# Optimization experiments

Hardware: AMD Instinct MI355X
Metric: run time of the kernel (lower is better)

The kernel has to match this reference:

```python
import jax, jax.numpy as jnp
import numpy as np

N_HEADS = 16
D_MODEL = 1024
NEG_INF = float('-inf')


def _rope_tables(seq_len, d_k, dtype):
    # RoPE(dim=d_k//2): Theta_i = 10000^(-i/dim), repeat-interleaved to width d_k;
    # positions start at 1 (torch uses arange(1, max_len+1)).
    dim = d_k // 2
    theta = jnp.exp(-jnp.arange(dim, dtype=dtype) * (np.log(10000.0) / dim))
    theta = jnp.repeat(theta, 2)                      # [d_k]
    pos = jnp.arange(1, seq_len + 1, dtype=dtype)[:, None]  # [S,1]
    ang = pos * theta                                 # [S,d_k]
    return jnp.sin(ang), jnp.cos(ang)


def _rope(x):
    # x: [B,H,S,d_k]; pair rotation (x0,x1)->(-x1,x0), Rx = x*cos + rot(x)*sin
    B, H, S, d_k = x.shape
    sin, cos = _rope_tables(S, d_k, x.dtype)
    xp = x.reshape(B, H, S, d_k // 2, 2)
    rot = jnp.stack([-xp[..., 1], xp[..., 0]], axis=-1).reshape(x.shape)
    return x * cos + rot * sin


def setup_inputs() -> dict:
    key = jax.random.key(0)
    ks = jax.random.split(key, 8)
    B, S, D, H = 2, 1024, D_MODEL, N_HEADS
    source_query = jax.random.normal(ks[0], (B, S, D), dtype=jnp.float32)
    source_key_value = jax.random.normal(ks[1], (B, S, D), dtype=jnp.float32)
    # tail padding: lengths in [820, 1024]
    q_len = jax.random.randint(ks[2], (B,), 820, S + 1)
    kv_len = jax.random.randint(ks[3], (B,), 820, S + 1)
    pos = jnp.arange(S)
    source_query_padding_mask = pos[None, :] >= q_len[:, None]    # True = pad
    source_key_value_padding_mask = pos[None, :] >= kv_len[:, None]
    prev = jax.random.normal(ks[4], (1, B, H, S, S), dtype=jnp.float32) * 0.5
    Wq = jax.random.normal(ks[5], (D, D), dtype=jnp.float32) * 0.02
    Wk = jax.random.normal(ks[6], (D, D), dtype=jnp.float32) * 0.02
    kv2 = jax.random.split(ks[7], 2)
    Wv = jax.random.normal(kv2[0], (D, D), dtype=jnp.float32) * 0.02
    Wproj = jax.random.normal(kv2[1], (D, D), dtype=jnp.float32) * 0.02
    return dict(source_query=source_query, source_key_value=source_key_value,
                source_query_padding_mask=source_query_padding_mask,
                source_key_value_padding_mask=source_key_value_padding_mask,
                prev=prev, Wq=Wq, Wk=Wk, Wv=Wv, Wproj=Wproj)


def reference(source_query, source_key_value, source_query_padding_mask,
              source_key_value_padding_mask, prev, Wq, Wk, Wv, Wproj):
    B, Sq, D = source_query.shape
    Sk = source_key_value.shape[1]
    H = N_HEADS
    d_k = D // H

    def split_heads(x, S):
        return x.reshape(B, S, H, d_k).transpose(0, 2, 1, 3)  # [B,H,S,d_k]

    # nn.Linear(bias=False): y = x @ W.T
    q = split_heads(jnp.einsum('bsd,ed->bse', source_query, Wq), Sq)
    k = split_heads(jnp.einsum('bsd,ed->bse', source_key_value, Wk), Sk)
    v = split_heads(jnp.einsum('bsd,ed->bse', source_key_value, Wv), Sk)

    q = _rope(q)
    k = _rope(k)

    scores = jnp.einsum('bhqd,bhkd->bhqk', q, k) * (d_k ** -0.5)
    q_pad = source_query_padding_mask[:, None, :, None]   # [B,1,Sq,1]
    kv_pad = source_key_value_padding_mask[:, None, None, :]  # [B,1,1,Sk]
    scores = jnp.where(q_pad, NEG_INF, scores)
    scores = jnp.where(kv_pad, NEG_INF, scores)
    causal = jnp.tril(jnp.ones((Sq, Sq), dtype=bool))      # masked=True
    scores = jnp.where(causal, scores, NEG_INF)

    prev_new = jnp.concatenate([prev, scores[None]], axis=0)  # [L+1,B,H,Sq,Sk]
    avg = prev_new.mean(0)

    # rows fully -inf (padded queries) would softmax to NaN in torch, then get
    # filled with 0 -> compute a safe softmax and zero those rows instead.
    safe = jnp.where(q_pad, 0.0, avg)
    w = jax.nn.softmax(safe, axis=-1)
    w = jnp.where(q_pad, 0.0, w)

    attn = jnp.einsum('bhqk,bhkd->bhqd', w, v)
    attn = attn.transpose(0, 2, 1, 3).reshape(B, Sq, D)
    out = jnp.einsum('bsd,ed->bse', attn, Wproj)  # dropout=0 (eval)
    return out, prev_new
```

## Files before the change

kernel.cpp:

```cpp
#include <hip/hip_runtime.h>
#include <math.h>

#define NSEQ 1024
#define NH   16
#define DKH  64

#define NEGBIG (-1.0e30f)

typedef unsigned short u16;
typedef unsigned int   u32;
typedef __attribute__((ext_vector_type(8))) short short8;
typedef __attribute__((ext_vector_type(4))) float f32x4;

__global__ __launch_bounds__(256) void normalize_masks(
    const unsigned char* __restrict__ qm, const unsigned char* __restrict__ km,
    int* __restrict__ outq, int* __restrict__ outk)
{
    __shared__ int flag;
    if (threadIdx.x == 0) flag = 0;
    __syncthreads();
    int f = 0;
    for (int i = threadIdx.x; i < 2048; i += 256) {
        if ((i & 3) && qm[i]) f = 1;
        if ((i & 3) && km[i]) f = 1;
    }
    if (f) atomicOr(&flag, 1);
    __syncthreads();
    const int isbyte = flag;
    for (int i = threadIdx.x; i < 2048; i += 256) {
        outq[i] = isbyte ? (int)qm[i] : ((const int*)qm)[i];
        outk[i] = isbyte ? (int)km[i] : ((const int*)km)[i];
    }
}

__device__ __forceinline__ u32 bf16_rn(float x) {
    u32 u = __float_as_uint(x);
    return (u + 0x7FFFu + ((u >> 16) & 1u)) >> 16;
}
__device__ __forceinline__ void bf16_split(float x, u32 &h, u32 &l) {
    h = bf16_rn(x);
    l = bf16_rn(x - __uint_as_float(h << 16));
}

__device__ __forceinline__ void mfma_core(
    const float* __restrict__ X, const float* __restrict__ W,
    u16 (*Ahi)[40], u16 (*Alo)[40], u16 (*Bhi)[40], u16 (*Blo)[40],
    f32x4 (&acc)[4][2], int m0, int e0, int tid)
{
    const int lane = tid & 63, wid = tid >> 6;
    const int wm = wid >> 1, wn = wid & 1;
    const int l15 = lane & 15, lq = lane >> 4;
    const int arow = tid >> 1, aks = (tid & 1) * 16;
    const int brow = tid >> 2, bks = (tid & 3) * 8;
    const float* aptr = &X[(size_t)(m0 + arow) * 1024 + aks];
    const float* bptr = &W[(size_t)(e0 + brow) * 1024 + bks];

    float4 xa[4], xb[2];
    #pragma unroll
    for (int c = 0; c < 4; ++c) xa[c] = *(const float4*)(aptr + 4 * c);
    #pragma unroll
    for (int c = 0; c < 2; ++c) xb[c] = *(const float4*)(bptr + 4 * c);

    for (int k0 = 0; k0 < 1024; k0 += 32) {
        u32 pah[8], pal[8], pbh[4], pbl[4];
        #pragma unroll
        for (int c = 0; c < 4; ++c) {
            u32 h0, l0, h1, l1, h2, l2, h3, l3;
            bf16_split(xa[c].x, h0, l0); bf16_split(xa[c].y, h1, l1);
            bf16_split(xa[c].z, h2, l2); bf16_split(xa[c].w, h3, l3);
            pah[2 * c] = h0 | (h1 << 16); pah[2 * c + 1] = h2 | (h3 << 16);
            pal[2 * c] = l0 | (l1 << 16); pal[2 * c + 1] = l2 | (l3 << 16);
        }
        #pragma unroll
        for (int c = 0; c < 2; ++c) {
            u32 h0, l0, h1, l1, h2, l2, h3, l3;
            bf16_split(xb[c].x, h0, l0); bf16_split(xb[c].y, h1, l1);
            bf16_split(xb[c].z, h2, l2); bf16_split(xb[c].w, h3, l3);
            pbh[2 * c] = h0 | (h1 << 16); pbh[2 * c + 1] = h2 | (h3 << 16);
            pbl[2 * c] = l0 | (l1 << 16); pbl[2 * c + 1] = l2 | (l3 << 16);
        }
        __syncthreads();
        *(uint4*)&Ahi[arow][aks]     = make_uint4(pah[0], pah[1], pah[2], pah[3]);
        *(uint4*)&Ahi[arow][aks + 8] = make_uint4(pah[4], pah[5], pah[6], pah[7]);
        *(uint4*)&Alo[arow][aks]     = make_uint4(pal[0], pal[1], pal[2], pal[3]);
        *(uint4*)&Alo[arow][aks + 8] = make_uint4(pal[4], pal[5], pal[6], pal[7]);
        *(uint4*)&Bhi[brow][bks]     = make_uint4(pbh[0], pbh[1], pbh[2], pbh[3]);
        *(uint4*)&Blo[brow][bks]     = make_uint4(pbl[0], pbl[1], pbl[2], pbl[3]);
        __syncthreads();
        if (k0 + 32 < 1024) {
            #pragma unroll
            for (int c = 0; c < 4; ++c) xa[c] = *(const float4*)(aptr + k0 + 32 + 4 * c);
            #pragma unroll
            for (int c = 0; c < 2; ++c) xb[c] = *(const float4*)(bptr + k0 + 32 + 4 * c);
        }
        short8 bh8[2], bl8[2];
        #pragma unroll
        for (int fn = 0; fn < 2; ++fn) {
            const int bc = wn * 32 + fn * 16 + l15;
            bh8[fn] = *(const short8*)&Bhi[bc][lq * 8];
            bl8[fn] = *(const short8*)&Blo[bc][lq * 8];
        }
        #pragma unroll
        for (int fm = 0; fm < 4; ++fm) {
            const int ar = wm * 64 + fm * 16 + l15;
            short8 ah8 = *(const short8*)&Ahi[ar][lq * 8];
            short8 al8 = *(const short8*)&Alo[ar][lq * 8];
            #pragma unroll
            for (int fn = 0; fn < 2; ++fn) {
                acc[fm][fn] = __builtin_amdgcn_mfma_f32_16x16x32_bf16(ah8, bh8[fn], acc[fm][fn], 0, 0, 0);
                acc[fm][fn] = __builtin_amdgcn_mfma_f32_16x16x32_bf16(ah8, bl8[fn], acc[fm][fn], 0, 0, 0);
                acc[fm][fn] = __builtin_amdgcn_mfma_f32_16x16x32_bf16(al8, bh8[fn], acc[fm][fn], 0, 0, 0);
            }
        }
    }
}

__global__ __launch_bounds__(256) void gemm_qkv(
    const float* __restrict__ srcq, const float* __restrict__ srckv,
    const float* __restrict__ Wq, const float* __restrict__ Wk,
    const float* __restrict__ Wv,
    float* __restrict__ qh, float* __restrict__ kh, float* __restrict__ vh)
{
    __shared__ __align__(16) u16 Ahi[128][40];
    __shared__ __align__(16) u16 Alo[128][40];
    __shared__ __align__(16) u16 Bhi[64][40];
    __shared__ __align__(16) u16 Blo[64][40];
    const int tid = threadIdx.x;
    const int z = blockIdx.z;
    const float* X = (z == 0) ? srcq : srckv;
    const float* W = (z == 0) ? Wq : (z == 1) ? Wk : Wv;
    float* Y       = (z == 0) ? qh : (z == 1) ? kh : vh;
    const int m0 = blockIdx.y * 128, e0 = blockIdx.x * 64;

    f32x4 acc[4][2];
    #pragma unroll
    for (int i = 0; i < 4; ++i)
        #pragma unroll
        for (int j = 0; j < 2; ++j) acc[i][j] = (f32x4){0.f, 0.f, 0.f, 0.f};

    mfma_core(X, W, Ahi, Alo, Bhi, Blo, acc, m0, e0, tid);

    const int lane = tid & 63, wid = tid >> 6;
    const int wm = wid >> 1, wn = wid & 1;
    const int l15 = lane & 15, lq = lane >> 4;
    const bool rope = (z != 2);
    const float cth = 0.28782313662425575f;
    float th[2];
    #pragma unroll
    for (int fn = 0; fn < 2; ++fn) {
        const int e = e0 + wn * 32 + fn * 16 + l15;
        th[fn] = rope ? expf(-(float)((e & 63) >> 1) * cth) : 0.f;
    }
    #pragma unroll
    for (int fm = 0; fm < 4; ++fm) {
        #pragma unroll
        for (int r = 0; r < 4; ++r) {
            const int m = m0 + wm * 64 + fm * 16 + lq * 4 + r;
            const int b = m >> 10, s = m & 1023;
            const float pos = (float)(s + 1);
            #pragma unroll
            for (int fn = 0; fn < 2; ++fn) {
                const int e = e0 + wn * 32 + fn * 16 + l15;
                float v = acc[fm][fn][r];
                const float vp = __shfl_xor(v, 1);
                if (rope) {
                    float sp, cp;
                    sincosf(pos * th[fn], &sp, &cp);
                    v = (lane & 1) ? (v * cp + vp * sp) : (v * cp - vp * sp);
                }
                const int h = e >> 6, db = e & 63;
                Y[(((size_t)(b * NH + h) << 10) + s) * DKH + db] = v;
            }
        }
    }
}

__global__ __launch_bounds__(256) void gemm_proj(
    const float* __restrict__ X, const float* __restrict__ W,
    float* __restrict__ Y)
{
    __shared__ __align__(16) u16 Ahi[128][40];
    __shared__ __align__(16) u16 Alo[128][40];
    __shared__ __align__(16) u16 Bhi[64][40];
    __shared__ __align__(16) u16 Blo[64][40];
    const int tid = threadIdx.x;
    const int m0 = blockIdx.y * 128, e0 = blockIdx.x * 64;

    f32x4 acc[4][2];
    #pragma unroll
    for (int i = 0; i < 4; ++i)
        #pragma unroll
        for (int j = 0; j < 2; ++j) acc[i][j] = (f32x4){0.f, 0.f, 0.f, 0.f};

    mfma_core(X, W, Ahi, Alo, Bhi, Blo, acc, m0, e0, tid);

    const int lane = tid & 63, wid = tid >> 6;
    const int wm = wid >> 1, wn = wid & 1;
    const int l15 = lane & 15, lq = lane >> 4;
    #pragma unroll
    for (int fm = 0; fm < 4; ++fm) {
        #pragma unroll
        for (int fn = 0; fn < 2; ++fn) {
            #pragma unroll
            for (int r = 0; r < 4; ++r) {
                const int row = m0 + wm * 64 + fm * 16 + lq * 4 + r;
                const int col = e0 + wn * 32 + fn * 16 + l15;
                Y[(size_t)row * 1024 + col] = acc[fm][fn][r];
            }
        }
    }
}

__global__ __launch_bounds__(256) void flash_fused(
    const float* __restrict__ qh, const float* __restrict__ kh,
    const float* __restrict__ vh, const float* __restrict__ prev,
    const int* __restrict__ nmq, const int* __restrict__ nmk,
    float* __restrict__ prevc, float* __restrict__ scb,
    float* __restrict__ attn)
{
    const int bh = blockIdx.y;
    const int b = bh >> 4, h = bh & 15;
    const int bx = blockIdx.x;
    const int qt = (bx & 1) ? (15 - (bx >> 1)) : (bx >> 1);
    const int q0 = qt * 64;
    const int tid = threadIdx.x;
    const int ti = tid >> 4, tj = tid & 15;
    const int r0 = ti * 4, c0 = tj * 4;
    const size_t base = ((size_t)bh << 10) * 1024;
    const float NI = NEGBIG;

    __shared__ float Qs[64][68];
    __shared__ float KW[64][68];
    __shared__ float Vs[64][68];

    const int lr = tid >> 2;
    const int ld0 = (tid & 3) * 4;
    {
        const float* qbase = qh + (((size_t)bh << 10) + q0) * DKH;
        #pragma unroll
        for (int dq = 0; dq < 4; ++dq) {
            const int d0 = ld0 + dq * 16;
            float4 qv = *(const float4*)&qbase[(size_t)lr * DKH + d0];
            Qs[d0 + 0][lr] = qv.x; Qs[d0 + 1][lr] = qv.y;
            Qs[d0 + 2][lr] = qv.z; Qs[d0 + 3][lr] = qv.w;
        }
    }

    {
        const float4 ninf4 = make_float4(NI, NI, NI, NI);
        for (int kt = qt + 1; kt < 16; ++kt) {
            const int k0 = kt * 64;
            #pragma unroll
            for (int u = 0; u < 4; ++u) {
                const int e = u * 256 + tid;
                const int rr = e >> 4, cc = (e & 15) * 4;
                const size_t idx = base + (size_t)(q0 + rr) * 1024 + k0 + cc;
                *(float4*)&prevc[idx] = *(const float4*)&prev[idx];
                *(float4*)&scb[idx] = ninf4;
            }
        }
    }

    int qmv[4];
    #pragma unroll
    for (int i = 0; i < 4; ++i) qmv[i] = nmq[(b << 10) + q0 + r0 + i];

    float m_i[4], l_i[4], O[4][4];
    #pragma unroll
    for (int i = 0; i < 4; ++i) {
        m_i[i] = -3.0e38f; l_i[i] = 0.f;
        #pragma unroll
        for (int j = 0; j < 4; ++j) O[i][j] = 0.f;
    }

    const float* kbase = kh + ((size_t)bh << 10) * DKH;
    const float* vbase = vh + ((size_t)bh << 10) * DKH;

    for (int kt = 0; kt <= qt; ++kt) {
        const int k0 = kt * 64;
        __syncthreads();

        #pragma unroll
        for (int dq = 0; dq < 4; ++dq) {
            const int d0 = ld0 + dq * 16;
            float4 kv4 = *(const float4*)&kbase[(size_t)(k0 + lr) * DKH + d0];
            KW[d0 + 0][lr] = kv4.x; KW[d0 + 1][lr] = kv4.y;
            KW[d0 + 2][lr] = kv4.z; KW[d0 + 3][lr] = kv4.w;
        }
        #pragma unroll
        for (int u = 0; u < 4; ++u) {
            const int e = u * 256 + tid;
            const int kv = e >> 4, dd = (e & 15) * 4;
            *(float4*)&Vs[kv][dd] =
                *(const float4*)&vbase[(size_t)(k0 + kv) * DKH + dd];
        }
        __syncthreads();

        float acc[4][4] = {{0.f}};
        #pragma unroll 8
        for (int d = 0; d < 64; ++d) {
            float a[4], bb[4];
            *(float4*)a  = *(const float4*)&Qs[d][r0];
            *(float4*)bb = *(const float4*)&KW[d][c0];
            #pragma unroll
            for (int i = 0; i < 4; ++i)
                #pragma unroll
                for (int j = 0; j < 4; ++j)
                    acc[i][j] += a[i] * bb[j];
        }

        int km[4];
        #pragma unroll
        for (int j = 0; j < 4; ++j) km[j] = nmk[(b << 10) + k0 + c0 + j];
        float aw[4][4], tmx[4];
        #pragma unroll
        for (int i = 0; i < 4; ++i) {
            const int row = q0 + r0 + i;
            float o[4];
            #pragma unroll
            for (int j = 0; j < 4; ++j) {
                const int col = k0 + c0 + j;
                const bool masked = (col > row) || (qmv[i] != 0) || (km[j] != 0);
                o[j] = masked ? NI : acc[i][j] * 0.125f;
            }
            const size_t idx = base + (size_t)row * 1024 + k0 + c0;
            *(float4*)&scb[idx] = make_float4(o[0], o[1], o[2], o[3]);
            const float4 p4 = *(const float4*)&prev[idx];
            *(float4*)&prevc[idx] = p4;
            aw[i][0] = 0.5f * (p4.x + o[0]);
            aw[i][1] = 0.5f * (p4.y + o[1]);
            aw[i][2] = 0.5f * (p4.z + o[2]);
            aw[i][3] = 0.5f * (p4.w + o[3]);
            tmx[i] = fmaxf(fmaxf(aw[i][0], aw[i][1]), fmaxf(aw[i][2], aw[i][3]));
        }
        #pragma unroll
        for (int i = 0; i < 4; ++i)
            #pragma unroll
            for (int off = 1; off < 16; off <<= 1)
                tmx[i] = fmaxf(tmx[i], __shfl_xor(tmx[i], off));

        __syncthreads();

        #pragma unroll
        for (int i = 0; i < 4; ++i) {
            const float mn = fmaxf(m_i[i], tmx[i]);
            const float fac = expf(m_i[i] - mn);
            m_i[i] = mn;
            float w0 = expf(aw[i][0] - mn);
            float w1 = expf(aw[i][1] - mn);
            float w2 = expf(aw[i][2] - mn);
            float w3 = expf(aw[i][3] - mn);
            float sl = w0 + w1 + w2 + w3;
            #pragma unroll
            for (int off = 1; off < 16; off <<= 1)
                sl += __shfl_xor(sl, off);
            l_i[i] = l_i[i] * fac + sl;
            #pragma unroll
            for (int j = 0; j < 4; ++j) O[i][j] *= fac;
            KW[c0 + 0][r0 + i] = w0;
            KW[c0 + 1][r0 + i] = w1;
            KW[c0 + 2][r0 + i] = w2;
            KW[c0 + 3][r0 + i] = w3;
        }
        __syncthreads();

        #pragma unroll 8
        for (int k = 0; k < 64; ++k) {
            float wv[4], vv[4];
            *(float4*)wv = *(const float4*)&KW[k][r0];
            *(float4*)vv = *(const float4*)&Vs[k][c0];
            #pragma unroll
            for (int i = 0; i < 4; ++i)
                #pragma unroll
                for (int j = 0; j < 4; ++j)
                    O[i][j] += wv[i] * vv[j];
        }
    }

    #pragma unroll
    for (int i = 0; i < 4; ++i) {
        const int q = q0 + r0 + i;
        const float inv = qmv[i] ? 0.f : 1.f / l_i[i];
        float4 o4 = make_float4(O[i][0] * inv, O[i][1] * inv,
                                O[i][2] * inv, O[i][3] * inv);
        *(float4*)&attn[(size_t)((b << 10) + q) * 1024 + (h << 6) + c0] = o4;
    }
}

extern "C" void kernel_launch(void* const* d_in, const int* in_sizes, int n_in,
                              void* d_out, int out_size, void* d_ws, size_t ws_size,
                              hipStream_t stream) {
    const float* srcq  = (const float*)d_in[0];
    const float* srckv = (const float*)d_in[1];
    const void*  qmask = d_in[2];
    const void*  kmask = d_in[3];
    const float* prev  = (const float*)d_in[4];
    const float* Wq    = (const float*)d_in[5];
    const float* Wk    = (const float*)d_in[6];
    const float* Wv    = (const float*)d_in[7];
    const float* Wp    = (const float*)d_in[8];

    float* out0  = (float*)d_out;
    float* prevc = out0 + 2097152;
    float* scb   = prevc + 33554432;

    float* qh   = (float*)d_ws;
    float* kh   = qh + 2097152;
    float* vh   = kh + 2097152;
    float* attn = vh + 2097152;
    int*   nmq  = (int*)(attn + 2097152);
    int*   nmk  = nmq + 2048;

    hipLaunchKernelGGL(normalize_masks, dim3(1), dim3(256), 0, stream,
                       (const unsigned char*)qmask, (const unsigned char*)kmask, nmq, nmk);
    hipLaunchKernelGGL(gemm_qkv, dim3(16, 16, 3), dim3(256), 0, stream,
                       srcq, srckv, Wq, Wk, Wv, qh, kh, vh);
    hipLaunchKernelGGL(flash_fused, dim3(16, 32), dim3(256), 0, stream,
                       qh, kh, vh, prev, nmq, nmk, prevc, scb, attn);
    hipLaunchKernelGGL(gemm_proj, dim3(16, 16), dim3(256), 0, stream,
                       attn, Wp, out0);
}
```

Baseline: 596.9 us.

## Pre-split inputs to bf16 hi/lo and move prev copy into a standalone kernel

Adds a pre-pass kernel that splits the activations and all four weight matrices into bf16 hi/lo arrays once. The GEMMs then load ready-made bf16 data instead of redoing the split in every tile, which removes repeated conversion work per block. The attention kernel now writes its output directly as bf16 hi/lo for the projection GEMM. The copy of prev into the output, and the fill of the fully masked upper blocks, move into a separate grid-stride kernel, so the fused attention kernel no longer carries that streaming traffic. The costs are extra kernel launches, more workspace, and a second full read of prev: once in the copy kernel and again in the attention kernel.

Result: slower. 648.0 us (+8.6%).

```diff
diff --git a/kernel.cpp b/kernel.cpp
--- a/kernel.cpp
+++ b/kernel.cpp
@@ -42,8 +42,56 @@
     l = bf16_rn(x - __uint_as_float(h << 16));
 }
 
+__global__ __launch_bounds__(256) void split_bf16(
+    const float* __restrict__ srcq, const float* __restrict__ srckv,
+    const float* __restrict__ Wq, const float* __restrict__ Wk,
+    const float* __restrict__ Wv, const float* __restrict__ Wp,
+    u16* __restrict__ sqh, u16* __restrict__ sql,
+    u16* __restrict__ skvh, u16* __restrict__ skvl,
+    u16* __restrict__ w4h, u16* __restrict__ w4l)
+{
+    const int z = blockIdx.z;
+    const float* src; u16 *dh, *dl; int n;
+    if (z == 0)      { src = srcq;  dh = sqh;  dl = sql;  n = 1 << 21; }
+    else if (z == 1) { src = srckv; dh = skvh; dl = skvl; n = 1 << 21; }
+    else {
+        src = (z == 2) ? Wq : (z == 3) ? Wk : (z == 4) ? Wv : Wp;
+        dh = w4h + ((size_t)(z - 2) << 20);
+        dl = w4l + ((size_t)(z - 2) << 20);
+        n = 1 << 20;
+    }
+    const int i8 = (blockIdx.x * 256 + threadIdx.x) * 8;
+    if (i8 >= n) return;
+    const float4 a = *(const float4*)&src[i8];
+    const float4 b = *(const float4*)&src[i8 + 4];
+    const float v[8] = {a.x, a.y, a.z, a.w, b.x, b.y, b.z, b.w};
+    u32 h[8], l[8];
+    #pragma unroll
+    for (int j = 0; j < 8; ++j) bf16_split(v[j], h[j], l[j]);
+    *(uint4*)&dh[i8] = make_uint4(h[0] | (h[1] << 16), h[2] | (h[3] << 16),
+                                  h[4] | (h[5] << 16), h[6] | (h[7] << 16));
+    *(uint4*)&dl[i8] = make_uint4(l[0] | (l[1] << 16), l[2] | (l[3] << 16),
+                                  l[4] | (l[5] << 16), l[6] | (l[7] << 16));
+}
+
+__global__ __launch_bounds__(256) void full_copy(
+    const float* __restrict__ prev, float* __restrict__ prevc,
+    float* __restrict__ scb)
+{
+    const float4 n4 = make_float4(NEGBIG, NEGBIG, NEGBIG, NEGBIG);
+    for (unsigned i = blockIdx.x * 256 + threadIdx.x; i < (1u << 23); i += gridDim.x * 256) {
+        const size_t e = (size_t)i * 4;
+        const float4 p = *(const float4*)&prev[e];
+        *(float4*)&prevc[e] = p;
+        const int q = (int)((e >> 10) & 1023);
+        const int k = (int)(e & 1023);
+        if ((k >> 6) > (q >> 6)) *(float4*)&scb[e] = n4;
+    }
+}
+
 __device__ __forceinline__ void mfma_core(
-    const float* __restrict__ X, const float* __restrict__ W,
+    const u16* __restrict__ Xhi, const u16* __restrict__ Xlo,
+    const u16* __restrict__ Whi, const u16* __restrict__ Wlo,
     u16 (*Ahi)[40], u16 (*Alo)[40], u16 (*Bhi)[40], u16 (*Blo)[40],
     f32x4 (&acc)[4][2], int m0, int e0, int tid)
 {
@@ -52,46 +100,34 @@
     const int l15 = lane & 15, lq = lane >> 4;
     const int arow = tid >> 1, aks = (tid & 1) * 16;
     const int brow = tid >> 2, bks = (tid & 3) * 8;
-    const float* aptr = &X[(size_t)(m0 + arow) * 1024 + aks];
-    const float* bptr = &W[(size_t)(e0 + brow) * 1024 + bks];
-
-    float4 xa[4], xb[2];
-    #pragma unroll
-    for (int c = 0; c < 4; ++c) xa[c] = *(const float4*)(aptr + 4 * c);
-    #pragma unroll
-    for (int c = 0; c < 2; ++c) xb[c] = *(const float4*)(bptr + 4 * c);
+    const u16* axh = &Xhi[(size_t)(m0 + arow) * 1024 + aks];
+    const u16* axl = &Xlo[(size_t)(m0 + arow) * 1024 + aks];
+    const u16* bxh = &Whi[(size_t)(e0 + brow) * 1024 + bks];
+    const u16* bxl = &Wlo[(size_t)(e0 + brow) * 1024 + bks];
+
+    uint4 rah0 = *(const uint4*)axh;
+    uint4 rah1 = *(const uint4*)(axh + 8);
+    uint4 ral0 = *(const uint4*)axl;
+    uint4 ral1 = *(const uint4*)(axl + 8);
+    uint4 rbh  = *(const uint4*)bxh;
+    uint4 rbl  = *(const uint4*)bxl;
 
     for (int k0 = 0; k0 < 1024; k0 += 32) {
-        u32 pah[8], pal[8], pbh[4], pbl[4];
-        #pragma unroll
-        for (int c = 0; c < 4; ++c) {
-            u32 h0, l0, h1, l1, h2, l2, h3, l3;
-            bf16_split(xa[c].x, h0, l0); bf16_split(xa[c].y, h1, l1);
-            bf16_split(xa[c].z, h2, l2); bf16_split(xa[c].w, h3, l3);
-            pah[2 * c] = h0 | (h1 << 16); pah[2 * c + 1] = h2 | (h3 << 16);
-            pal[2 * c] = l0 | (l1 << 16); pal[2 * c + 1] = l2 | (l3 << 16);
-        }
-        #pragma unroll
-        for (int c = 0; c < 2; ++c) {
-            u32 h0, l0, h1, l1, h2, l2, h3, l3;
-            bf16_split(xb[c].x, h0, l0); bf16_split(xb[c].y, h1, l1);
-            bf16_split(xb[c].z, h2, l2); bf16_split(xb[c].w, h3, l3);
-            pbh[2 * c] = h0 | (h1 << 16); pbh[2 * c + 1] = h2 | (h3 << 16);
-            pbl[2 * c] = l0 | (l1 << 16); pbl[2 * c + 1] = l2 | (l3 << 16);
-        }
-        __syncthreads();
-        *(uint4*)&Ahi[arow][aks]     = make_uint4(pah[0], pah[1], pah[2], pah[3]);
-        *(uint4*)&Ahi[arow][aks + 8] = make_uint4(pah[4], pah[5], pah[6], pah[7]);
-        *(uint4*)&Alo[arow][aks]     = make_uint4(pal[0], pal[1], pal[2], pal[3]);
-        *(uint4*)&Alo[arow][aks + 8] = make_uint4(pal[4], pal[5], pal[6], pal[7]);
-        *(uint4*)&Bhi[brow][bks]     = make_uint4(pbh[0], pbh[1], pbh[2], pbh[3]);
-        *(uint4*)&Blo[brow][bks]     = make_uint4(pbl[0], pbl[1], pbl[2], pbl[3]);
+        __syncthreads();
+        *(uint4*)&Ahi[arow][aks]     = rah0;
+        *(uint4*)&Ahi[arow][aks + 8] = rah1;
+        *(uint4*)&Alo[arow][aks]     = ral0;
+        *(uint4*)&Alo[arow][aks + 8] = ral1;
+        *(uint4*)&Bhi[brow][bks]     = rbh;
+        *(uint4*)&Blo[brow][bks]     = rbl;
         __syncthreads();
         if (k0 + 32 < 1024) {
-            #pragma unroll
-            for (int c = 0; c < 4; ++c) xa[c] = *(const float4*)(aptr + k0 + 32 + 4 * c);
-            #pragma unroll
-            for (int c = 0; c < 2; ++c) xb[c] = *(const float4*)(bptr + k0 + 32 + 4 * c);
+            rah0 = *(const uint4*)(axh + k0 + 32);
+            rah1 = *(const uint4*)(axh + k0 + 40);
+            ral0 = *(const uint4*)(axl + k0 + 32);
+            ral1 = *(const uint4*)(axl + k0 + 40);
+            rbh  = *(const uint4*)(bxh + k0 + 32);
+            rbl  = *(const uint4*)(bxl + k0 + 32);
         }
         short8 bh8[2], bl8[2];
         #pragma unroll
@@ -116,9 +152,9 @@
 }
 
 __global__ __launch_bounds__(256) void gemm_qkv(
-    const float* __restrict__ srcq, const float* __restrict__ srckv,
-    const float* __restrict__ Wq, const float* __restrict__ Wk,
-    const float* __restrict__ Wv,
+    const u16* __restrict__ sqh, const u16* __restrict__ sql,
+    const u16* __restrict__ skvh, const u16* __restrict__ skvl,
+    const u16* __restrict__ w4h, const u16* __restrict__ w4l,
     float* __restrict__ qh, float* __restrict__ kh, float* __restrict__ vh)
 {
     __shared__ __align__(16) u16 Ahi[128][40];
@@ -127,9 +163,11 @@
     __shared__ __align__(16) u16 Blo[64][40];
     const int tid = threadIdx.x;
     const int z = blockIdx.z;
-    const float* X = (z == 0) ? srcq : srckv;
-    const float* W = (z == 0) ? Wq : (z == 1) ? Wk : Wv;
-    float* Y       = (z == 0) ? qh : (z == 1) ? kh : vh;
+    const u16* Xhi = (z == 0) ? sqh : skvh;
+    const u16* Xlo = (z == 0) ? sql : skvl;
+    const u16* Whi = w4h + ((size_t)z << 20);
+    const u16* Wlo = w4l + ((size_t)z << 20);
+    float* Y = (z == 0) ? qh : (z == 1) ? kh : vh;
     const int m0 = blockIdx.y * 128, e0 = blockIdx.x * 64;
 
     f32x4 acc[4][2];
@@ -138,7 +176,7 @@
         #pragma unroll
         for (int j = 0; j < 2; ++j) acc[i][j] = (f32x4){0.f, 0.f, 0.f, 0.f};
 
-    mfma_core(X, W, Ahi, Alo, Bhi, Blo, acc, m0, e0, tid);
+    mfma_core(Xhi, Xlo, Whi, Wlo, Ahi, Alo, Bhi, Blo, acc, m0, e0, tid);
 
     const int lane = tid & 63, wid = tid >> 6;
     const int wm = wid >> 1, wn = wid & 1;
@@ -168,15 +206,16 @@
                     sincosf(pos * th[fn], &sp, &cp);
                     v = (lane & 1) ? (v * cp + vp * sp) : (v * cp - vp * sp);
                 }
-                const int h = e >> 6, db = e & 63;
-                Y[(((size_t)(b * NH + h) << 10) + s) * DKH + db] = v;
+                const int hh = e >> 6, db = e & 63;
+                Y[(((size_t)(b * NH + hh) << 10) + s) * DKH + db] = v;
             }
         }
     }
 }
 
 __global__ __launch_bounds__(256) void gemm_proj(
-    const float* __restrict__ X, const float* __restrict__ W,
+    const u16* __restrict__ atnh, const u16* __restrict__ atnl,
+    const u16* __restrict__ wph, const u16* __restrict__ wpl,
     float* __restrict__ Y)
 {
     __shared__ __align__(16) u16 Ahi[128][40];
@@ -192,7 +231,7 @@
         #pragma unroll
         for (int j = 0; j < 2; ++j) acc[i][j] = (f32x4){0.f, 0.f, 0.f, 0.f};
 
-    mfma_core(X, W, Ahi, Alo, Bhi, Blo, acc, m0, e0, tid);
+    mfma_core(atnh, atnl, wph, wpl, Ahi, Alo, Bhi, Blo, acc, m0, e0, tid);
 
     const int lane = tid & 63, wid = tid >> 6;
     const int wm = wid >> 1, wn = wid & 1;
@@ -215,8 +254,7 @@
     const float* __restrict__ qh, const float* __restrict__ kh,
     const float* __restrict__ vh, const float* __restrict__ prev,
     const int* __restrict__ nmq, const int* __restrict__ nmk,
-    float* __restrict__ prevc, float* __restrict__ scb,
-    float* __restrict__ attn)
+    float* __restrict__ scb, u16* __restrict__ atnh, u16* __restrict__ atnl)
 {
     const int bh = blockIdx.y;
     const int b = bh >> 4, h = bh & 15;
@@ -246,21 +284,6 @@
         }
     }
 
-    {
-        const float4 ninf4 = make_float4(NI, NI, NI, NI);
-        for (int kt = qt + 1; kt < 16; ++kt) {
-            const int k0 = kt * 64;
-            #pragma unroll
-            for (int u = 0; u < 4; ++u) {
-                const int e = u * 256 + tid;
-                const int rr = e >> 4, cc = (e & 15) * 4;
-                const size_t idx = base + (size_t)(q0 + rr) * 1024 + k0 + cc;
-                *(float4*)&prevc[idx] = *(const float4*)&prev[idx];
-                *(float4*)&scb[idx] = ninf4;
-            }
-        }
-    }
-
     int qmv[4];
     #pragma unroll
     for (int i = 0; i < 4; ++i) qmv[i] = nmq[(b << 10) + q0 + r0 + i];
@@ -326,7 +349,6 @@
             const size_t idx = base + (size_t)row * 1024 + k0 + c0;
             *(float4*)&scb[idx] = make_float4(o[0], o[1], o[2], o[3]);
             const float4 p4 = *(const float4*)&prev[idx];
-            *(float4*)&prevc[idx] = p4;
             aw[i][0] = 0.5f * (p4.x + o[0]);
             aw[i][1] = 0.5f * (p4.y + o[1]);
             aw[i][2] = 0.5f * (p4.z + o[2]);
@@ -381,9 +403,14 @@
     for (int i = 0; i < 4; ++i) {
         const int q = q0 + r0 + i;
         const float inv = qmv[i] ? 0.f : 1.f / l_i[i];
-        float4 o4 = make_float4(O[i][0] * inv, O[i][1] * inv,
-                                O[i][2] * inv, O[i][3] * inv);
-        *(float4*)&attn[(size_t)((b << 10) + q) * 1024 + (h << 6) + c0] = o4;
+        u32 sh0, sl0, sh1, sl1, sh2, sl2, sh3, sl3;
+        bf16_split(O[i][0] * inv, sh0, sl0);
+        bf16_split(O[i][1] * inv, sh1, sl1);
+        bf16_split(O[i][2] * inv, sh2, sl2);
+        bf16_split(O[i][3] * inv, sh3, sl3);
+        const size_t aidx = (size_t)((b << 10) + q) * 1024 + (h << 6) + c0;
+        *(uint2*)&atnh[aidx] = make_uint2(sh0 | (sh1 << 16), sh2 | (sh3 << 16));
+        *(uint2*)&atnl[aidx] = make_uint2(sl0 | (sl1 << 16), sl2 | (sl3 << 16));
     }
 }
 
@@ -407,16 +434,28 @@
     float* qh   = (float*)d_ws;
     float* kh   = qh + 2097152;
     float* vh   = kh + 2097152;
-    float* attn = vh + 2097152;
-    int*   nmq  = (int*)(attn + 2097152);
-    int*   nmk  = nmq + 2048;
+    u16* atnh = (u16*)(vh + 2097152);
+    u16* atnl = atnh + 2097152;
+    u16* sqh  = atnl + 2097152;
+    u16* sql  = sqh + 2097152;
+    u16* skvh = sql + 2097152;
+    u16* skvl = skvh + 2097152;
+    u16* w4h  = skvl + 2097152;
+    u16* w4l  = w4h + 4194304;
+    int* nmq  = (int*)(w4l + 4194304);
+    int* nmk  = nmq + 2048;
 
     hipLaunchKernelGGL(normalize_masks, dim3(1), dim3(256), 0, stream,
                        (const unsigned char*)qmask, (const unsigned char*)kmask, nmq, nmk);
+    hipLaunchKernelGGL(split_bf16, dim3(1024, 1, 6), dim3(256), 0, stream,
+                       srcq, srckv, Wq, Wk, Wv, Wp,
+                       sqh, sql, skvh, skvl, w4h, w4l);
     hipLaunchKernelGGL(gemm_qkv, dim3(16, 16, 3), dim3(256), 0, stream,
-                       srcq, srckv, Wq, Wk, Wv, qh, kh, vh);
+                       sqh, sql, skvh, skvl, w4h, w4l, qh, kh, vh);
+    hipLaunchKernelGGL(full_copy, dim3(2048), dim3(256), 0, stream,
+                       prev, prevc, scb);
     hipLaunchKernelGGL(flash_fused, dim3(16, 32), dim3(256), 0, stream,
-                       qh, kh, vh, prev, nmq, nmk, prevc, scb, attn);
+                       qh, kh, vh, prev, nmq, nmk, scb, atnh, atnl);
     hipLaunchKernelGGL(gemm_proj, dim3(16, 16), dim3(256), 0, stream,
-                       attn, Wp, out0);
-}
+                       atnh, atnl, w4h + 3145728, w4l + 3145728, out0);
+}
```
